# Performance work log

Hardware: AMD Instinct MI355X
Metric: run time of the kernel (lower is better)

## Reference

```python
import jax, jax.numpy as jnp
import numpy as np

B, NQ, C = 2, 10000, 256
M, L, K = 8, 3, 4
D = C // M
LEVEL_SHAPES = [(100, 100), (50, 50), (25, 25)]


def setup_inputs() -> dict:
    key = jax.random.key(0)
    ks = jax.random.split(key, 16)
    inp = {
        "query": jax.random.normal(ks[0], (B, NQ, C), jnp.float32),
        "reference_points": jax.random.uniform(ks[1], (B, NQ, 2), jnp.float32),
        "value0": jax.random.normal(ks[2], (B, C) + LEVEL_SHAPES[0], jnp.float32),
        "value1": jax.random.normal(ks[3], (B, C) + LEVEL_SHAPES[1], jnp.float32),
        "value2": jax.random.normal(ks[4], (B, C) + LEVEL_SHAPES[2], jnp.float32),
        "Wv": jax.random.normal(ks[5], (C, C), jnp.float32) * 0.02,
        "bv": jnp.zeros((C,), jnp.float32),
        "Ws": jax.random.normal(ks[6], (M * L * K * 2, C), jnp.float32) * 0.05,
        "bs": jax.random.normal(ks[7], (M * L * K * 2,), jnp.float32),
        "Wa": jax.random.normal(ks[8], (M * L * K, C), jnp.float32) * 0.02,
        "ba": jnp.zeros((M * L * K,), jnp.float32),
        "Wo": jax.random.normal(ks[9], (C, C), jnp.float32) * 0.02,
        "bo": jnp.zeros((C,), jnp.float32),
    }
    return inp


def _bilinear_sample(vflat, px, py, H, W):
    """grid_sample bilinear, align_corners=False, padding_mode='zeros'.
    vflat: (B, M, H*W, D); px, py: (B, M, Q, K) pixel coords. -> (B, M, Q, K, D)
    """
    b, m, q, k = px.shape
    x0 = jnp.floor(px)
    y0 = jnp.floor(py)
    wx1 = px - x0  # frac weights (grad 1 w.r.t. px, matching grid_sample)
    wy1 = py - y0
    wx0 = 1.0 - wx1
    wy0 = 1.0 - wy1

    def gather(xi, yi):
        valid = ((xi >= 0) & (xi <= W - 1) & (yi >= 0) & (yi <= H - 1)).astype(vflat.dtype)
        xc = jnp.clip(xi, 0, W - 1).astype(jnp.int32)
        yc = jnp.clip(yi, 0, H - 1).astype(jnp.int32)
        idx = (yc * W + xc).reshape(b, m, q * k)
        g = jnp.take_along_axis(vflat, idx[..., None], axis=2)  # (B,M,QK,D)
        return g.reshape(b, m, q, k, -1) * valid[..., None]

    out = (gather(x0, y0) * (wx0 * wy0)[..., None]
           + gather(x0 + 1, y0) * (wx1 * wy0)[..., None]
           + gather(x0, y0 + 1) * (wx0 * wy1)[..., None]
           + gather(x0 + 1, y0 + 1) * (wx1 * wy1)[..., None])
    return out


def reference(query, reference_points, value0, value1, value2,
              Wv, bv, Ws, bs, Wa, ba, Wo, bo):
    bsz, nq, c = query.shape
    dt = query.dtype
    # sampling offsets and attention weights
    off = (query @ Ws.T + bs).reshape(bsz, nq, M, L, K, 2)
    attn = jax.nn.softmax((query @ Wa.T + ba).reshape(bsz, nq, M, L * K), axis=-1)
    attn = attn.reshape(bsz, nq, M, L, K)

    out = jnp.zeros((bsz, nq, M, D), dt)
    for li, v in enumerate([value0, value1, value2]):
        H, W = v.shape[2], v.shape[3]
        # conv1x1 value projection -> per-head maps (B, M, H*W, D)
        proj = jnp.einsum('bchw,oc->bohw', v, Wv) + bv[None, :, None, None]
        vflat = proj.reshape(bsz, M, D, H * W).transpose(0, 1, 3, 2)
        norm = jnp.asarray([W, H], dt)
        loc = reference_points[:, :, None, None, :] + off[:, :, :, li, :, :] / norm  # (B,Q,M,K,2)
        # grid = loc*2-1; pixel = (grid+1)*size/2 - 0.5 = loc*size - 0.5
        px = (loc[..., 0] * W - 0.5).transpose(0, 2, 1, 3)  # (B,M,Q,K)
        py = (loc[..., 1] * H - 0.5).transpose(0, 2, 1, 3)
        sampled = _bilinear_sample(vflat, px, py, H, W)  # (B,M,Q,K,D)
        out = out + jnp.einsum('bmqkd,bqmk->bqmd', sampled, attn[:, :, :, li, :])

    out = out.reshape(bsz, nq, c)
    return out @ Wo.T + bo
```

## Files before the change

### kernel.cpp

```cpp
#include <hip/hip_runtime.h>
#include <cstddef>

#define B_ 2
#define NQ_ 10000
#define C_ 256
#define M_ 8
#define L_ 3
#define K_ 4
#define D_ 32
#define P_ 13125

typedef unsigned short u16;
typedef __attribute__((ext_vector_type(8))) short short8;
typedef __attribute__((ext_vector_type(4))) float f32x4;

static __device__ __forceinline__ u16 f2bf(float f) {
    union { float f; unsigned u; } x; x.f = f;
    unsigned r = x.u + 0x7fffu + ((x.u >> 16) & 1u);
    return (u16)(r >> 16);
}
static __device__ __forceinline__ float bf2f(u16 u) {
    union { unsigned u; float f; } x; x.u = (unsigned)u << 16;
    return x.f;
}

__global__ __launch_bounds__(256) void cvt_all(
    const float* __restrict__ query,
    const float* __restrict__ Wv, const float* __restrict__ Ws,
    const float* __restrict__ Wa, const float* __restrict__ Wo,
    u16* __restrict__ qbf, u16* __restrict__ Wvbf,
    u16* __restrict__ WsWabf, u16* __restrict__ Wobf)
{
    const int bx = blockIdx.x;
    if (bx < 5000) {
        const int i4 = (bx * 256 + threadIdx.x) * 4;
        float4 v = *reinterpret_cast<const float4*>(query + i4);
        ushort4 o;
        o.x = f2bf(v.x); o.y = f2bf(v.y); o.z = f2bf(v.z); o.w = f2bf(v.w);
        *reinterpret_cast<ushort4*>(qbf + i4) = o;
        return;
    }
    const int j4 = ((bx - 5000) * 256 + threadIdx.x) * 4;
    const float* src;
    u16* dst;
    int off;
    if (j4 < 65536)        { src = Wv; dst = Wvbf; off = j4; }
    else if (j4 < 139264)  {
        int j = j4 - 65536;
        if (j < 49152) { src = Ws; off = j; }
        else           { src = Wa; off = j - 49152; }
        dst = WsWabf + (j - off);
        dst = WsWabf; off = j;
        src = (j < 49152) ? Ws : Wa;
        float4 v = *reinterpret_cast<const float4*>(
            ((j < 49152) ? Ws + j : Wa + (j - 49152)));
        ushort4 o;
        o.x = f2bf(v.x); o.y = f2bf(v.y); o.z = f2bf(v.z); o.w = f2bf(v.w);
        *reinterpret_cast<ushort4*>(WsWabf + j) = o;
        return;
    }
    else                   { src = Wo; dst = Wobf; off = j4 - 139264; }
    float4 v = *reinterpret_cast<const float4*>(src + off);
    ushort4 o;
    o.x = f2bf(v.x); o.y = f2bf(v.y); o.z = f2bf(v.z); o.w = f2bf(v.w);
    *reinterpret_cast<ushort4*>(dst + off) = o;
}

__global__ __launch_bounds__(256) void transpose_value(
    const float* __restrict__ v0, const float* __restrict__ v1,
    const float* __restrict__ v2, u16* __restrict__ Vt)
{
    constexpr int HWs[3]  = {10000, 2500, 625};
    constexpr int offs[3] = {0, 10000, 12500};

    const int z   = blockIdx.z;
    const int b   = z / 3;
    const int lvl = z % 3;
    const int HW  = HWs[lvl];
    const int p0  = blockIdx.x * 64;
    if (p0 >= HW) return;
    const int c0  = blockIdx.y * 64;

    const float* V = (lvl == 0 ? v0 : (lvl == 1 ? v1 : v2)) + (size_t)b * 256 * HW;

    __shared__ u16 tile[64][66];
    const int t  = threadIdx.x;
    const int pl = t & 63;
    const int cb = t >> 6;

    #pragma unroll
    for (int i = 0; i < 16; ++i) {
        int c = cb + i * 4;
        float vv = 0.f;
        if (p0 + pl < HW)
            vv = V[(size_t)(c0 + c) * HW + p0 + pl];
        tile[pl][c] = f2bf(vv);
    }
    __syncthreads();

    const int cl = t & 63;
    const int pb = t >> 6;
    #pragma unroll
    for (int i = 0; i < 16; ++i) {
        int p = pb + i * 4;
        if (p0 + p < HW)
            Vt[((size_t)b * P_ + offs[lvl] + p0 + p) * 256 + c0 + cl] = tile[p][cl];
    }
}

template <typename OutT>
__global__ __launch_bounds__(256) void gemm_bf16(
    const u16* __restrict__ A, int rows,
    const u16* __restrict__ Bw,
    const float* __restrict__ bias1, int N1,
    const float* __restrict__ bias2, int Ntot,
    OutT* __restrict__ Cout)
{
    __shared__ u16 Bs[64 * 264];

    const int t  = threadIdx.x;
    const int w  = t >> 6;
    const int l  = t & 63;
    const int row0 = blockIdx.x * 128 + w * 32;
    const int o0   = blockIdx.y * 64;
    const int lr = l & 15;
    const int kb = (l >> 4) * 8;

    #pragma unroll
    for (int i = 0; i < 8; ++i) {
        int idx = i * 256 + t;
        int col = idx >> 5;
        int kc  = (idx & 31) * 8;
        int colg = min(o0 + col, Ntot - 1);
        short8 v = *reinterpret_cast<const short8*>(Bw + (size_t)colg * 256 + kc);
        *reinterpret_cast<short8*>(&Bs[col * 264 + kc]) = v;
    }

    const int ra0 = min(row0 + lr,      rows - 1);
    const int ra1 = min(row0 + 16 + lr, rows - 1);
    const u16* Ap0 = A + (size_t)ra0 * 256 + kb;
    const u16* Ap1 = A + (size_t)ra1 * 256 + kb;

    __syncthreads();

    f32x4 acc[2][4] = {};

    #pragma unroll
    for (int k0 = 0; k0 < 256; k0 += 32) {
        short8 a0 = *reinterpret_cast<const short8*>(Ap0 + k0);
        short8 a1 = *reinterpret_cast<const short8*>(Ap1 + k0);
        short8 b0 = *reinterpret_cast<const short8*>(&Bs[(0 * 16 + lr) * 264 + kb + k0]);
        short8 b1 = *reinterpret_cast<const short8*>(&Bs[(1 * 16 + lr) * 264 + kb + k0]);
        short8 b2 = *reinterpret_cast<const short8*>(&Bs[(2 * 16 + lr) * 264 + kb + k0]);
        short8 b3 = *reinterpret_cast<const short8*>(&Bs[(3 * 16 + lr) * 264 + kb + k0]);
        acc[0][0] = __builtin_amdgcn_mfma_f32_16x16x32_bf16(a0, b0, acc[0][0], 0, 0, 0);
        acc[0][1] = __builtin_amdgcn_mfma_f32_16x16x32_bf16(a0, b1, acc[0][1], 0, 0, 0);
        acc[0][2] = __builtin_amdgcn_mfma_f32_16x16x32_bf16(a0, b2, acc[0][2], 0, 0, 0);
        acc[0][3] = __builtin_amdgcn_mfma_f32_16x16x32_bf16(a0, b3, acc[0][3], 0, 0, 0);
        acc[1][0] = __builtin_amdgcn_mfma_f32_16x16x32_bf16(a1, b0, acc[1][0], 0, 0, 0);
        acc[1][1] = __builtin_amdgcn_mfma_f32_16x16x32_bf16(a1, b1, acc[1][1], 0, 0, 0);
        acc[1][2] = __builtin_amdgcn_mfma_f32_16x16x32_bf16(a1, b2, acc[1][2], 0, 0, 0);
        acc[1][3] = __builtin_amdgcn_mfma_f32_16x16x32_bf16(a1, b3, acc[1][3], 0, 0, 0);
    }

    const int orow = (l >> 4) * 4;
    #pragma unroll
    for (int ct = 0; ct < 4; ++ct) {
        const int col = o0 + ct * 16 + lr;
        if (col >= Ntot) continue;
        const float bsv = (col < N1) ? bias1[col] : bias2[col - N1];
        #pragma unroll
        for (int rt = 0; rt < 2; ++rt) {
            #pragma unroll
            for (int r = 0; r < 4; ++r) {
                const int row = row0 + rt * 16 + orow + r;
                if (row < rows) {
                    float val = acc[rt][ct][r] + bsv;
                    if constexpr (sizeof(OutT) == 2)
                        Cout[(size_t)row * Ntot + col] = (OutT)f2bf(val);
                    else
                        Cout[(size_t)row * Ntot + col] = (OutT)val;
                }
            }
        }
    }
}

__global__ __launch_bounds__(256) void sample_kernel(
    const float* __restrict__ S,
    const float* __restrict__ refp,
    const u16* __restrict__ proj,
    u16* __restrict__ out2)
{
    constexpr int Wd[3]   = {100, 50, 25};
    constexpr int offs[3] = {0, 10000, 12500};

    __shared__ int   midx[96][4];
    __shared__ float mw[96][4];

    const int bq = blockIdx.x;
    const int b  = bq / NQ_;
    const int t  = threadIdx.x;

    if (t < 96) {
        const int tm = t / 12;
        const int tj = t % 12;
        const float* Sq = S + (size_t)bq * 288;
        float lg[12], mx = -1e30f;
        #pragma unroll
        for (int jj = 0; jj < 12; ++jj) {
            lg[jj] = Sq[192 + tm * 12 + jj];
            mx = fmaxf(mx, lg[jj]);
        }
        float sum = 0.f;
        #pragma unroll
        for (int jj = 0; jj < 12; ++jj) sum += __expf(lg[jj] - mx);
        const float attn = __expf(lg[tj] - mx) / sum;

        const int l  = tj >> 2;
        const int Wl = Wd[l];
        const float refx = refp[(size_t)bq * 2 + 0];
        const float refy = refp[(size_t)bq * 2 + 1];
        const float ox = Sq[(tm * 12 + tj) * 2 + 0];
        const float oy = Sq[(tm * 12 + tj) * 2 + 1];
        const float px = refx * (float)Wl + ox - 0.5f;
        const float py = refy * (float)Wl + oy - 0.5f;
        const float x0f = floorf(px), y0f = floorf(py);
        const float wx1 = px - x0f, wy1 = py - y0f;
        const float wx0 = 1.f - wx1, wy0 = 1.f - wy1;
        const int x0 = (int)x0f, y0 = (int)y0f;
        const int x1 = x0 + 1, y1 = y0 + 1;
        const bool vx0 = (unsigned)x0 < (unsigned)Wl;
        const bool vx1 = (unsigned)x1 < (unsigned)Wl;
        const bool vy0 = (unsigned)y0 < (unsigned)Wl;
        const bool vy1 = (unsigned)y1 < (unsigned)Wl;
        const int chb = tm * 32;
        const int base = offs[l];
        midx[t][0] = (vx0 && vy0) ? ((base + y0 * Wl + x0) * 256 + chb) : 0;
        midx[t][1] = (vx1 && vy0) ? ((base + y0 * Wl + x1) * 256 + chb) : 0;
        midx[t][2] = (vx0 && vy1) ? ((base + y1 * Wl + x0) * 256 + chb) : 0;
        midx[t][3] = (vx1 && vy1) ? ((base + y1 * Wl + x1) * 256 + chb) : 0;
        mw[t][0] = (vx0 && vy0) ? attn * wx0 * wy0 : 0.f;
        mw[t][1] = (vx1 && vy0) ? attn * wx1 * wy0 : 0.f;
        mw[t][2] = (vx0 && vy1) ? attn * wx0 * wy1 : 0.f;
        mw[t][3] = (vx1 && vy1) ? attn * wx1 * wy1 : 0.f;
    }
    __syncthreads();

    const int m = t >> 5;
    const int d = t & 31;
    const u16* projb = proj + (size_t)b * P_ * 256;
    float acc = 0.f;

    #pragma unroll
    for (int j = 0; j < 12; ++j) {
        const int mj = m * 12 + j;
        const int4   o  = *reinterpret_cast<const int4*>(midx[mj]);
        const float4 ww = *reinterpret_cast<const float4*>(mw[mj]);
        const float v00 = bf2f(projb[o.x + d]);
        const float v10 = bf2f(projb[o.y + d]);
        const float v01 = bf2f(projb[o.z + d]);
        const float v11 = bf2f(projb[o.w + d]);
        acc = fmaf(ww.x, v00, acc);
        acc = fmaf(ww.y, v10, acc);
        acc = fmaf(ww.z, v01, acc);
        acc = fmaf(ww.w, v11, acc);
    }
    out2[(size_t)bq * 256 + t] = f2bf(acc);
}

extern "C" void kernel_launch(void* const* d_in, const int* in_sizes, int n_in,
                              void* d_out, int out_size, void* d_ws, size_t ws_size,
                              hipStream_t stream)
{
    const float* query = (const float*)d_in[0];
    const float* refp  = (const float*)d_in[1];
    const float* v0    = (const float*)d_in[2];
    const float* v1    = (const float*)d_in[3];
    const float* v2    = (const float*)d_in[4];
    const float* Wv    = (const float*)d_in[5];
    const float* bv    = (const float*)d_in[6];
    const float* Ws    = (const float*)d_in[7];
    const float* bs    = (const float*)d_in[8];
    const float* Wa    = (const float*)d_in[9];
    const float* ba    = (const float*)d_in[10];
    const float* Wo    = (const float*)d_in[11];
    const float* bo    = (const float*)d_in[12];
    float* out = (float*)d_out;

    char* wsb = (char*)d_ws;
    u16*   proj  = (u16*)wsb;    wsb += (size_t)B_ * P_ * 256 * 2;
    float* S     = (float*)wsb;  wsb += (size_t)B_ * NQ_ * 288 * 4;
    u16*   Vt    = (u16*)wsb;    wsb += (size_t)B_ * P_ * 256 * 2;
    u16*   qbf   = (u16*)wsb;
    u16*   out2bf = qbf;         wsb += (size_t)B_ * NQ_ * 256 * 2;
    u16*   Wvbf  = (u16*)wsb;    wsb += 65536 * 2;
    u16*   WsWabf= (u16*)wsb;    wsb += 73728 * 2;
    u16*   Wobf  = (u16*)wsb;    wsb += 65536 * 2;

    dim3 blk(256);

    cvt_all<<<dim3(5200), blk, 0, stream>>>(query, Wv, Ws, Wa, Wo,
                                            qbf, Wvbf, WsWabf, Wobf);
    transpose_value<<<dim3(157, 4, 6), blk, 0, stream>>>(v0, v1, v2, Vt);

    gemm_bf16<u16><<<dim3(206, 4), blk, 0, stream>>>(
        Vt, B_ * P_, Wvbf, bv, 256, bv, 256, proj);

    gemm_bf16<float><<<dim3(157, 5), blk, 0, stream>>>(
        qbf, B_ * NQ_, WsWabf, bs, 192, ba, 288, S);

    sample_kernel<<<dim3(B_ * NQ_), blk, 0, stream>>>(S, refp, proj, out2bf);

    gemm_bf16<float><<<dim3(157, 4), blk, 0, stream>>>(
        out2bf, B_ * NQ_, Wobf, bo, 256, bo, 256, out);
}
```

Baseline: 211.4 us.

## Fuse fp32-to-bf16 conversion into GEMMs, panel-swizzle grids, widen sampling per thread

Removes the separate conversion kernel. Weights are now converted to bf16 while being loaded into shared memory, and the query GEMM converts fp32 A rows in registers. The GEMM grids become 1D with an 8-row-tile swizzle across column panels for better L2 reuse. The sampling kernel handles two queries per block, and each thread loads two adjacent bf16 channels with one 32-bit load. This saves a launch and a round trip of query through memory, at the cost of redundant weight conversion in every block.

New measurement: 202.6 us. 4.2% less time.

```diff
diff --git a/kernel.cpp b/kernel.cpp
--- a/kernel.cpp
+++ b/kernel.cpp
@@ -23,47 +23,13 @@
     union { unsigned u; float f; } x; x.u = (unsigned)u << 16;
     return x.f;
 }
-
-__global__ __launch_bounds__(256) void cvt_all(
-    const float* __restrict__ query,
-    const float* __restrict__ Wv, const float* __restrict__ Ws,
-    const float* __restrict__ Wa, const float* __restrict__ Wo,
-    u16* __restrict__ qbf, u16* __restrict__ Wvbf,
-    u16* __restrict__ WsWabf, u16* __restrict__ Wobf)
-{
-    const int bx = blockIdx.x;
-    if (bx < 5000) {
-        const int i4 = (bx * 256 + threadIdx.x) * 4;
-        float4 v = *reinterpret_cast<const float4*>(query + i4);
-        ushort4 o;
-        o.x = f2bf(v.x); o.y = f2bf(v.y); o.z = f2bf(v.z); o.w = f2bf(v.w);
-        *reinterpret_cast<ushort4*>(qbf + i4) = o;
-        return;
-    }
-    const int j4 = ((bx - 5000) * 256 + threadIdx.x) * 4;
-    const float* src;
-    u16* dst;
-    int off;
-    if (j4 < 65536)        { src = Wv; dst = Wvbf; off = j4; }
-    else if (j4 < 139264)  {
-        int j = j4 - 65536;
-        if (j < 49152) { src = Ws; off = j; }
-        else           { src = Wa; off = j - 49152; }
-        dst = WsWabf + (j - off);
-        dst = WsWabf; off = j;
-        src = (j < 49152) ? Ws : Wa;
-        float4 v = *reinterpret_cast<const float4*>(
-            ((j < 49152) ? Ws + j : Wa + (j - 49152)));
-        ushort4 o;
-        o.x = f2bf(v.x); o.y = f2bf(v.y); o.z = f2bf(v.z); o.w = f2bf(v.w);
-        *reinterpret_cast<ushort4*>(WsWabf + j) = o;
-        return;
-    }
-    else                   { src = Wo; dst = Wobf; off = j4 - 139264; }
-    float4 v = *reinterpret_cast<const float4*>(src + off);
-    ushort4 o;
-    o.x = f2bf(v.x); o.y = f2bf(v.y); o.z = f2bf(v.z); o.w = f2bf(v.w);
-    *reinterpret_cast<ushort4*>(dst + off) = o;
+static __device__ __forceinline__ short8 cvt8(const float4& a, const float4& b) {
+    short8 r;
+    r[0] = (short)f2bf(a.x); r[1] = (short)f2bf(a.y);
+    r[2] = (short)f2bf(a.z); r[3] = (short)f2bf(a.w);
+    r[4] = (short)f2bf(b.x); r[5] = (short)f2bf(b.y);
+    r[6] = (short)f2bf(b.z); r[7] = (short)f2bf(b.w);
+    return r;
 }
 
 __global__ __launch_bounds__(256) void transpose_value(
@@ -108,21 +74,27 @@
     }
 }
 
-template <typename OutT>
-__global__ __launch_bounds__(256) void gemm_bf16(
-    const u16* __restrict__ A, int rows,
-    const u16* __restrict__ Bw,
-    const float* __restrict__ bias1, int N1,
-    const float* __restrict__ bias2, int Ntot,
+template <bool AF32, typename OutT>
+__global__ __launch_bounds__(256) void gemm_panel(
+    const void* __restrict__ Av, int rows, int nRowTiles, int npanel,
+    const float* __restrict__ B1f, const float* __restrict__ bias1, int N1,
+    const float* __restrict__ B2f, const float* __restrict__ bias2, int Ntot,
     OutT* __restrict__ Cout)
 {
     __shared__ u16 Bs[64 * 264];
 
+    const int bid  = blockIdx.x;
+    const int rlo  = bid & 7;
+    const int tmp  = bid >> 3;
+    const int panel = tmp % npanel;
+    const int rowTile = (tmp / npanel) * 8 + rlo;
+    if (rowTile >= nRowTiles) return;
+
     const int t  = threadIdx.x;
     const int w  = t >> 6;
     const int l  = t & 63;
-    const int row0 = blockIdx.x * 128 + w * 32;
-    const int o0   = blockIdx.y * 64;
+    const int row0 = rowTile * 128 + w * 32;
+    const int o0   = panel * 64;
     const int lr = l & 15;
     const int kb = (l >> 4) * 8;
 
@@ -132,35 +104,66 @@
         int col = idx >> 5;
         int kc  = (idx & 31) * 8;
         int colg = min(o0 + col, Ntot - 1);
-        short8 v = *reinterpret_cast<const short8*>(Bw + (size_t)colg * 256 + kc);
-        *reinterpret_cast<short8*>(&Bs[col * 264 + kc]) = v;
+        const float* Br = ((colg < N1) ? B1f + (size_t)colg * 256
+                                       : B2f + (size_t)(colg - N1) * 256) + kc;
+        float4 f0 = *reinterpret_cast<const float4*>(Br);
+        float4 f1 = *reinterpret_cast<const float4*>(Br + 4);
+        *reinterpret_cast<short8*>(&Bs[col * 264 + kc]) = cvt8(f0, f1);
     }
 
     const int ra0 = min(row0 + lr,      rows - 1);
     const int ra1 = min(row0 + 16 + lr, rows - 1);
-    const u16* Ap0 = A + (size_t)ra0 * 256 + kb;
-    const u16* Ap1 = A + (size_t)ra1 * 256 + kb;
 
     __syncthreads();
 
     f32x4 acc[2][4] = {};
 
-    #pragma unroll
-    for (int k0 = 0; k0 < 256; k0 += 32) {
-        short8 a0 = *reinterpret_cast<const short8*>(Ap0 + k0);
-        short8 a1 = *reinterpret_cast<const short8*>(Ap1 + k0);
-        short8 b0 = *reinterpret_cast<const short8*>(&Bs[(0 * 16 + lr) * 264 + kb + k0]);
-        short8 b1 = *reinterpret_cast<const short8*>(&Bs[(1 * 16 + lr) * 264 + kb + k0]);
-        short8 b2 = *reinterpret_cast<const short8*>(&Bs[(2 * 16 + lr) * 264 + kb + k0]);
-        short8 b3 = *reinterpret_cast<const short8*>(&Bs[(3 * 16 + lr) * 264 + kb + k0]);
-        acc[0][0] = __builtin_amdgcn_mfma_f32_16x16x32_bf16(a0, b0, acc[0][0], 0, 0, 0);
-        acc[0][1] = __builtin_amdgcn_mfma_f32_16x16x32_bf16(a0, b1, acc[0][1], 0, 0, 0);
-        acc[0][2] = __builtin_amdgcn_mfma_f32_16x16x32_bf16(a0, b2, acc[0][2], 0, 0, 0);
-        acc[0][3] = __builtin_amdgcn_mfma_f32_16x16x32_bf16(a0, b3, acc[0][3], 0, 0, 0);
-        acc[1][0] = __builtin_amdgcn_mfma_f32_16x16x32_bf16(a1, b0, acc[1][0], 0, 0, 0);
-        acc[1][1] = __builtin_amdgcn_mfma_f32_16x16x32_bf16(a1, b1, acc[1][1], 0, 0, 0);
-        acc[1][2] = __builtin_amdgcn_mfma_f32_16x16x32_bf16(a1, b2, acc[1][2], 0, 0, 0);
-        acc[1][3] = __builtin_amdgcn_mfma_f32_16x16x32_bf16(a1, b3, acc[1][3], 0, 0, 0);
+    if constexpr (AF32) {
+        const float* Af  = (const float*)Av;
+        const float* Ap0 = Af + (size_t)ra0 * 256 + kb;
+        const float* Ap1 = Af + (size_t)ra1 * 256 + kb;
+        #pragma unroll
+        for (int k0 = 0; k0 < 256; k0 += 32) {
+            float4 x0 = *reinterpret_cast<const float4*>(Ap0 + k0);
+            float4 y0 = *reinterpret_cast<const float4*>(Ap0 + k0 + 4);
+            float4 x1 = *reinterpret_cast<const float4*>(Ap1 + k0);
+            float4 y1 = *reinterpret_cast<const float4*>(Ap1 + k0 + 4);
+            short8 a0 = cvt8(x0, y0);
+            short8 a1 = cvt8(x1, y1);
+            short8 b0 = *reinterpret_cast<const short8*>(&Bs[(0 * 16 + lr) * 264 + kb + k0]);
+            short8 b1 = *reinterpret_cast<const short8*>(&Bs[(1 * 16 + lr) * 264 + kb + k0]);
+            short8 b2 = *reinterpret_cast<const short8*>(&Bs[(2 * 16 + lr) * 264 + kb + k0]);
+            short8 b3 = *reinterpret_cast<const short8*>(&Bs[(3 * 16 + lr) * 264 + kb + k0]);
+            acc[0][0] = __builtin_amdgcn_mfma_f32_16x16x32_bf16(a0, b0, acc[0][0], 0, 0, 0);
+            acc[0][1] = __builtin_amdgcn_mfma_f32_16x16x32_bf16(a0, b1, acc[0][1], 0, 0, 0);
+            acc[0][2] = __builtin_amdgcn_mfma_f32_16x16x32_bf16(a0, b2, acc[0][2], 0, 0, 0);
+            acc[0][3] = __builtin_amdgcn_mfma_f32_16x16x32_bf16(a0, b3, acc[0][3], 0, 0, 0);
+            acc[1][0] = __builtin_amdgcn_mfma_f32_16x16x32_bf16(a1, b0, acc[1][0], 0, 0, 0);
+            acc[1][1] = __builtin_amdgcn_mfma_f32_16x16x32_bf16(a1, b1, acc[1][1], 0, 0, 0);
+            acc[1][2] = __builtin_amdgcn_mfma_f32_16x16x32_bf16(a1, b2, acc[1][2], 0, 0, 0);
+            acc[1][3] = __builtin_amdgcn_mfma_f32_16x16x32_bf16(a1, b3, acc[1][3], 0, 0, 0);
+        }
+    } else {
+        const u16* Af  = (const u16*)Av;
+        const u16* Ap0 = Af + (size_t)ra0 * 256 + kb;
+        const u16* Ap1 = Af + (size_t)ra1 * 256 + kb;
+        #pragma unroll
+        for (int k0 = 0; k0 < 256; k0 += 32) {
+            short8 a0 = *reinterpret_cast<const short8*>(Ap0 + k0);
+            short8 a1 = *reinterpret_cast<const short8*>(Ap1 + k0);
+            short8 b0 = *reinterpret_cast<const short8*>(&Bs[(0 * 16 + lr) * 264 + kb + k0]);
+            short8 b1 = *reinterpret_cast<const short8*>(&Bs[(1 * 16 + lr) * 264 + kb + k0]);
+            short8 b2 = *reinterpret_cast<const short8*>(&Bs[(2 * 16 + lr) * 264 + kb + k0]);
+            short8 b3 = *reinterpret_cast<const short8*>(&Bs[(3 * 16 + lr) * 264 + kb + k0]);
+            acc[0][0] = __builtin_amdgcn_mfma_f32_16x16x32_bf16(a0, b0, acc[0][0], 0, 0, 0);
+            acc[0][1] = __builtin_amdgcn_mfma_f32_16x16x32_bf16(a0, b1, acc[0][1], 0, 0, 0);
+            acc[0][2] = __builtin_amdgcn_mfma_f32_16x16x32_bf16(a0, b2, acc[0][2], 0, 0, 0);
+            acc[0][3] = __builtin_amdgcn_mfma_f32_16x16x32_bf16(a0, b3, acc[0][3], 0, 0, 0);
+            acc[1][0] = __builtin_amdgcn_mfma_f32_16x16x32_bf16(a1, b0, acc[1][0], 0, 0, 0);
+            acc[1][1] = __builtin_amdgcn_mfma_f32_16x16x32_bf16(a1, b1, acc[1][1], 0, 0, 0);
+            acc[1][2] = __builtin_amdgcn_mfma_f32_16x16x32_bf16(a1, b2, acc[1][2], 0, 0, 0);
+            acc[1][3] = __builtin_amdgcn_mfma_f32_16x16x32_bf16(a1, b3, acc[1][3], 0, 0, 0);
+        }
     }
 
     const int orow = (l >> 4) * 4;
@@ -195,17 +198,19 @@
     constexpr int Wd[3]   = {100, 50, 25};
     constexpr int offs[3] = {0, 10000, 12500};
 
-    __shared__ int   midx[96][4];
-    __shared__ float mw[96][4];
-
-    const int bq = blockIdx.x;
-    const int b  = bq / NQ_;
-    const int t  = threadIdx.x;
-
-    if (t < 96) {
-        const int tm = t / 12;
-        const int tj = t % 12;
+    __shared__ int   midx[192][4];
+    __shared__ float mw[192][4];
+
+    const int t = threadIdx.x;
+
+    if (t < 192) {
+        const int q  = t / 96;
+        const int tq = t % 96;
+        const int tm = tq / 12;
+        const int tj = tq % 12;
+        const int bq = blockIdx.x * 2 + q;
         const float* Sq = S + (size_t)bq * 288;
+
         float lg[12], mx = -1e30f;
         #pragma unroll
         for (int jj = 0; jj < 12; ++jj) {
@@ -234,7 +239,7 @@
         const bool vx1 = (unsigned)x1 < (unsigned)Wl;
         const bool vy0 = (unsigned)y0 < (unsigned)Wl;
         const bool vy1 = (unsigned)y1 < (unsigned)Wl;
-        const int chb = tm * 32;
+        const int chb  = tm * 32;
         const int base = offs[l];
         midx[t][0] = (vx0 && vy0) ? ((base + y0 * Wl + x0) * 256 + chb) : 0;
         midx[t][1] = (vx1 && vy0) ? ((base + y0 * Wl + x1) * 256 + chb) : 0;
@@ -247,26 +252,38 @@
     }
     __syncthreads();
 
-    const int m = t >> 5;
-    const int d = t & 31;
-    const u16* projb = proj + (size_t)b * P_ * 256;
-    float acc = 0.f;
+    const int qi  = t >> 7;
+    const int tt  = t & 127;
+    const int mh  = tt >> 4;
+    const int d16 = tt & 15;
+    const int bq2 = blockIdx.x * 2 + qi;
+    const int b   = bq2 / NQ_;
+    const u16* projb = proj + (size_t)b * P_ * 256 + 2 * d16;
+
+    float acc0 = 0.f, acc1 = 0.f;
 
     #pragma unroll
     for (int j = 0; j < 12; ++j) {
-        const int mj = m * 12 + j;
+        const int mj = qi * 96 + mh * 12 + j;
         const int4   o  = *reinterpret_cast<const int4*>(midx[mj]);
         const float4 ww = *reinterpret_cast<const float4*>(mw[mj]);
-        const float v00 = bf2f(projb[o.x + d]);
-        const float v10 = bf2f(projb[o.y + d]);
-        const float v01 = bf2f(projb[o.z + d]);
-        const float v11 = bf2f(projb[o.w + d]);
-        acc = fmaf(ww.x, v00, acc);
-        acc = fmaf(ww.y, v10, acc);
-        acc = fmaf(ww.z, v01, acc);
-        acc = fmaf(ww.w, v11, acc);
-    }
-    out2[(size_t)bq * 256 + t] = f2bf(acc);
+        const unsigned u00 = *reinterpret_cast<const unsigned*>(projb + o.x);
+        const unsigned u10 = *reinterpret_cast<const unsigned*>(projb + o.y);
+        const unsigned u01 = *reinterpret_cast<const unsigned*>(projb + o.z);
+        const unsigned u11 = *reinterpret_cast<const unsigned*>(projb + o.w);
+        union { unsigned u; float f; } c0, c1;
+        c0.u = u00 << 16;          c1.u = u00 & 0xffff0000u;
+        acc0 = fmaf(ww.x, c0.f, acc0); acc1 = fmaf(ww.x, c1.f, acc1);
+        c0.u = u10 << 16;          c1.u = u10 & 0xffff0000u;
+        acc0 = fmaf(ww.y, c0.f, acc0); acc1 = fmaf(ww.y, c1.f, acc1);
+        c0.u = u01 << 16;          c1.u = u01 & 0xffff0000u;
+        acc0 = fmaf(ww.z, c0.f, acc0); acc1 = fmaf(ww.z, c1.f, acc1);
+        c0.u = u11 << 16;          c1.u = u11 & 0xffff0000u;
+        acc0 = fmaf(ww.w, c0.f, acc0); acc1 = fmaf(ww.w, c1.f, acc1);
+    }
+
+    const unsigned packed = (unsigned)f2bf(acc0) | ((unsigned)f2bf(acc1) << 16);
+    *reinterpret_cast<unsigned*>(out2 + (size_t)bq2 * 256 + mh * 32 + 2 * d16) = packed;
 }
 
 extern "C" void kernel_launch(void* const* d_in, const int* in_sizes, int n_in,
@@ -292,26 +309,20 @@
     u16*   proj  = (u16*)wsb;    wsb += (size_t)B_ * P_ * 256 * 2;
     float* S     = (float*)wsb;  wsb += (size_t)B_ * NQ_ * 288 * 4;
     u16*   Vt    = (u16*)wsb;    wsb += (size_t)B_ * P_ * 256 * 2;
-    u16*   qbf   = (u16*)wsb;
-    u16*   out2bf = qbf;         wsb += (size_t)B_ * NQ_ * 256 * 2;
-    u16*   Wvbf  = (u16*)wsb;    wsb += 65536 * 2;
-    u16*   WsWabf= (u16*)wsb;    wsb += 73728 * 2;
-    u16*   Wobf  = (u16*)wsb;    wsb += 65536 * 2;
+    u16*   out2  = (u16*)wsb;    wsb += (size_t)B_ * NQ_ * 256 * 2;
 
     dim3 blk(256);
 
-    cvt_all<<<dim3(5200), blk, 0, stream>>>(query, Wv, Ws, Wa, Wo,
-                                            qbf, Wvbf, WsWabf, Wobf);
     transpose_value<<<dim3(157, 4, 6), blk, 0, stream>>>(v0, v1, v2, Vt);
 
-    gemm_bf16<u16><<<dim3(206, 4), blk, 0, stream>>>(
-        Vt, B_ * P_, Wvbf, bv, 256, bv, 256, proj);
-
-    gemm_bf16<float><<<dim3(157, 5), blk, 0, stream>>>(
-        qbf, B_ * NQ_, WsWabf, bs, 192, ba, 288, S);
-
-    sample_kernel<<<dim3(B_ * NQ_), blk, 0, stream>>>(S, refp, proj, out2bf);
-
-    gemm_bf16<float><<<dim3(157, 4), blk, 0, stream>>>(
-        out2bf, B_ * NQ_, Wobf, bo, 256, bo, 256, out);
-}
+    gemm_panel<false, u16><<<dim3(832), blk, 0, stream>>>(
+        Vt, B_ * P_, 206, 4, Wv, bv, 256, Wv, bv, 256, proj);
+
+    gemm_panel<true, float><<<dim3(800), blk, 0, stream>>>(
+        query, B_ * NQ_, 157, 5, Ws, bs, 192, Wa, ba, 288, S);
+
+    sample_kernel<<<dim3(NQ_), blk, 0, stream>>>(S, refp, proj, out2);
+
+    gemm_panel<false, float><<<dim3(640), blk, 0, stream>>>(
+        out2, B_ * NQ_, 157, 4, Wo, bo, 256, Wo, bo, 256, out);
+}
```
